# Kernel tuning notes

Measured on AMD Instinct MI355X. Metric: run time of the kernel, lower is better.

The kernel has to match this reference:

```python
import math
import jax, jax.numpy as jnp
import numpy as np
from jax import lax

B, C, H, W = 4, 256, 64, 64
TD = 256
GROUPS = 32
EPS = 1e-5


def group_norm(x, scale, bias, groups=GROUPS, eps=EPS):
    b, c, h, w = x.shape
    xg = x.reshape(b, groups, c // groups, h, w)
    m = xg.mean(axis=(2, 3, 4), keepdims=True)
    v = xg.var(axis=(2, 3, 4), keepdims=True)
    xn = ((xg - m) * lax.rsqrt(v + eps)).reshape(b, c, h, w)
    return xn * scale[None, :, None, None] + bias[None, :, None, None]


def conv3x3(x, w, b):
    y = lax.conv_general_dilated(x, w, (1, 1), 'SAME',
                                 dimension_numbers=('NCHW', 'OIHW', 'NCHW'))
    return y + b[None, :, None, None]


def setup_inputs() -> dict:
    key = jax.random.key(0)
    ks = jax.random.split(key, 10)
    s = 0.02
    return {
        'x': jax.random.normal(ks[0], (B, C, H, W), jnp.float32),
        'time_embed': jax.random.normal(ks[1], (B, TD), jnp.float32),
        # ResNetBlock params
        'gn1_s': jnp.ones((C,), jnp.float32), 'gn1_b': jnp.zeros((C,), jnp.float32),
        'conv1_w': jax.random.normal(ks[2], (C, C, 3, 3), jnp.float32) * s,
        'conv1_b': jnp.zeros((C,), jnp.float32),
        'mlp_w': jax.random.normal(ks[3], (2 * C, TD), jnp.float32) * s,
        'mlp_b': jnp.zeros((2 * C,), jnp.float32),
        'gn2_s': jnp.ones((C,), jnp.float32), 'gn2_b': jnp.zeros((C,), jnp.float32),
        'conv2_w': jax.random.normal(ks[4], (C, C, 3, 3), jnp.float32) * s,
        'conv2_b': jnp.zeros((C,), jnp.float32),
        # SelfAttention params (n_head=1, 1x1 convs stored as matrices)
        'gnA_s': jnp.ones((C,), jnp.float32), 'gnA_b': jnp.zeros((C,), jnp.float32),
        'qkv_w': jax.random.normal(ks[5], (3 * C, C), jnp.float32) * s,
        'out_w': jax.random.normal(ks[6], (C, C), jnp.float32) * s,
        'out_b': jnp.zeros((C,), jnp.float32),
    }


def reference(x, time_embed, gn1_s, gn1_b, conv1_w, conv1_b, mlp_w, mlp_b,
              gn2_s, gn2_b, conv2_w, conv2_b, gnA_s, gnA_b, qkv_w, out_w, out_b):
    # --- ResNetBlock ---
    h = conv3x3(jax.nn.silu(group_norm(x, gn1_s, gn1_b)), conv1_w, conv1_b)
    # time-embedding FiLM: SiLU -> Linear -> (gamma, beta)
    gb = jnp.dot(jax.nn.silu(time_embed), mlp_w.T) + mlp_b  # [B, 2C]
    gamma, beta = jnp.split(gb[:, :, None, None], 2, axis=1)
    h = (1.0 + gamma) * h + beta
    h = conv3x3(jax.nn.silu(group_norm(h, gn2_s, gn2_b)), conv2_w, conv2_b)
    xr = h + x  # res_conv is Identity since dim == dim_out

    # --- SelfAttention (n_head=1, scale = sqrt(channel)) ---
    b, c, hh, ww = xr.shape
    n = group_norm(xr, gnA_s, gnA_b)
    qkv = jnp.einsum('oc,bchw->bohw', qkv_w, n)  # [B, 3C, H, W]
    q, k, v = jnp.split(qkv.reshape(b, 3 * c, hh * ww), 3, axis=1)  # [B,C,HW] each
    attn = jnp.einsum('bcs,bct->bst', q, k) / math.sqrt(c)  # [B, HW, HW]
    attn = jax.nn.softmax(attn, axis=-1)
    o = jnp.einsum('bst,bct->bcs', attn, v).reshape(b, c, hh, ww)
    o = jnp.einsum('oc,bchw->bohw', out_w, o) + out_b[None, :, None, None]
    return o + xr
```

## Files before the change

kernel.cpp:

```cpp
#include <hip/hip_runtime.h>
#include <math.h>

#define SS 4096
#define NE 4194304

typedef __attribute__((ext_vector_type(8))) short short8;
typedef __attribute__((ext_vector_type(4))) short short4v;
typedef __attribute__((ext_vector_type(4))) float f32x4;
typedef __attribute__((ext_vector_type(16))) float f32x16;

__device__ __forceinline__ float wave_sum(float v) {
#pragma unroll
  for (int off = 32; off > 0; off >>= 1) v += __shfl_xor(v, off, 64);
  return v;
}
__device__ __forceinline__ float silu_f(float y) { return y / (1.f + __expf(-y)); }

__device__ __forceinline__ unsigned short to_bf(float x) {
  union { float f; unsigned u; } v; v.f = x;
  unsigned r = v.u + 0x7FFFu + ((v.u >> 16) & 1u);
  return (unsigned short)(r >> 16);
}
__device__ __forceinline__ float bf2f(short s) {
  union { unsigned u; float f; } v;
  v.u = ((unsigned)(unsigned short)s) << 16;
  return v.f;
}

__global__ __launch_bounds__(256) void gn_stats_k(const float* __restrict__ x,
                                                  float* __restrict__ stats) {
  const float4* p = (const float4*)(x + (size_t)blockIdx.x * 32768);
  float s = 0.f, q = 0.f;
  for (int i = threadIdx.x; i < 8192; i += 256) {
    float4 v = p[i];
    s += v.x + v.y + v.z + v.w;
    q += v.x * v.x + v.y * v.y + v.z * v.z + v.w * v.w;
  }
  s = wave_sum(s); q = wave_sum(q);
  __shared__ float red[8];
  int wid = threadIdx.x >> 6;
  if ((threadIdx.x & 63) == 0) { red[wid] = s; red[wid + 4] = q; }
  __syncthreads();
  if (threadIdx.x == 0) {
    s = red[0] + red[1] + red[2] + red[3];
    q = red[4] + red[5] + red[6] + red[7];
    float m = s * (1.f / 32768.f);
    float var = q * (1.f / 32768.f) - m * m;
    stats[blockIdx.x * 2] = m;
    stats[blockIdx.x * 2 + 1] = rsqrtf(var + 1e-5f);
  }
}

template <int DO_SILU>
__global__ __launch_bounds__(256) void gn_t_k(const float* __restrict__ x,
    const float* __restrict__ stats, const float* __restrict__ sc,
    const float* __restrict__ bi, short* __restrict__ G) {
  __shared__ short T[64][72];
  const int tid = threadIdx.x;
  const int st = blockIdx.x & 63;
  const int ct = (blockIdx.x >> 6) & 3;
  const int b = blockIdx.x >> 8;
  const int s0 = st * 64, c0 = ct * 64;
#pragma unroll
  for (int r = 0; r < 4; ++r) {
    int idx = r * 256 + tid;
    int c_l = idx >> 4, s4 = idx & 15;
    int c = c0 + c_l;
    int sidx = (b * 32 + (c >> 3)) * 2;
    float m = stats[sidx], rs = stats[sidx + 1];
    float a = sc[c] * rs;
    float t = bi[c] - m * a;
    float4 v = *(const float4*)(x + ((size_t)(b * 256 + c)) * 4096 + s0 + s4 * 4);
    float o0 = v.x * a + t, o1 = v.y * a + t, o2 = v.z * a + t, o3 = v.w * a + t;
    if (DO_SILU) { o0 = silu_f(o0); o1 = silu_f(o1); o2 = silu_f(o2); o3 = silu_f(o3); }
    T[s4 * 4 + 0][c_l] = (short)to_bf(o0);
    T[s4 * 4 + 1][c_l] = (short)to_bf(o1);
    T[s4 * 4 + 2][c_l] = (short)to_bf(o2);
    T[s4 * 4 + 3][c_l] = (short)to_bf(o3);
  }
  __syncthreads();
#pragma unroll
  for (int r = 0; r < 2; ++r) {
    int idx = r * 256 + tid;
    int s_l = idx >> 3, cg = idx & 7;
    *(short8*)(G + ((size_t)(b * 4096 + s0 + s_l)) * 256 + c0 + cg * 8) =
        *(const short8*)&T[s_l][cg * 8];
  }
}

__global__ __launch_bounds__(256) void prep_k(
    const float* __restrict__ conv1_w, const float* __restrict__ conv2_w,
    const float* __restrict__ qkv_w, const float* __restrict__ out_w,
    const float* __restrict__ te, const float* __restrict__ mlp_w,
    const float* __restrict__ mlp_b, short* __restrict__ Wt1,
    short* __restrict__ Wt2, short* __restrict__ wqb, short* __restrict__ wob,
    float* __restrict__ gbuf) {
  const int bid = blockIdx.x, tid = threadIdx.x;
  if (bid < 512) {
    __shared__ short L[9][256];
    const float* w = (bid < 256) ? conv1_w : conv2_w;
    short* wt = (bid < 256) ? Wt1 : Wt2;
    const int oc = bid & 255;
    const float* wp = w + (size_t)oc * 2304;
    for (int i = tid; i < 2304; i += 256) {
      int ic = i / 9, t = i - ic * 9;
      L[t][ic] = (short)to_bf(wp[i]);
    }
    __syncthreads();
    for (int i = tid; i < 2304; i += 256) {
      int t = i >> 8, ic = i & 255;
      wt[((size_t)(t * 256 + oc)) * 256 + ic] = L[t][ic];
    }
  } else if (bid < 1280) {
    int row = bid - 512;
    float sc = (row < 256) ? 0.0625f : 1.f;
    wqb[(size_t)row * 256 + tid] = (short)to_bf(qkv_w[(size_t)row * 256 + tid] * sc);
  } else if (bid < 1536) {
    int row = bid - 1280;
    wob[(size_t)row * 256 + tid] = (short)to_bf(out_w[(size_t)row * 256 + tid]);
  } else {
    int t2 = (bid - 1536) * 256 + tid;
    int b = t2 >> 9, jj = t2 & 511;
    const float* tp = te + b * 256;
    const float* wp = mlp_w + jj * 256;
    float acc = mlp_b[jj];
    for (int t = 0; t < 256; ++t) acc += silu_f(tp[t]) * wp[t];
    gbuf[t2] = acc;
  }
}

__device__ __forceinline__ short8 ld2x4(const short* p) {
  short4v lo = *(const short4v*)p;
  short4v hi = *(const short4v*)(p + 4);
  short8 r;
  r[0] = lo[0]; r[1] = lo[1]; r[2] = lo[2]; r[3] = lo[3];
  r[4] = hi[0]; r[5] = hi[1]; r[6] = hi[2]; r[7] = hi[3];
  return r;
}

template <int MODE>
__global__ __launch_bounds__(256, 1) void conv_mfma_k(
    const short* __restrict__ G, const short* __restrict__ Wt,
    const float* __restrict__ bias, const float* __restrict__ gb,
    const float* __restrict__ resid, float* __restrict__ out) {
  __shared__ __align__(16) short Xs[6][66][36];
  __shared__ __align__(16) short Ws[9][64][32];
  const int tid = threadIdx.x;
  const int oc0 = (blockIdx.x & 3) * 64;
  const int oy = ((blockIdx.x >> 2) & 15) * 4;
  const int b = blockIdx.x >> 6;
  const int wv = tid >> 6, lane = tid & 63;
  const int ln = lane & 31, hf = lane >> 5;

  f32x16 O00 = {}, O01 = {}, O10 = {}, O11 = {};

  for (int ic0 = 0; ic0 < 256; ic0 += 32) {
    __syncthreads();
    for (int i = tid; i < 1584; i += 256) {
      int r = i / 264;
      int rem = i - r * 264;
      int col = rem >> 2, g = rem & 3;
      int gy = oy + r - 1, gx = col - 1;
      short4v lo = {0, 0, 0, 0}, hi = {0, 0, 0, 0};
      if ((unsigned)gy < 64u && (unsigned)gx < 64u) {
        const short* gp = G + ((size_t)(b * 4096 + gy * 64 + gx)) * 256 + ic0 + g * 8;
        lo = *(const short4v*)gp;
        hi = *(const short4v*)(gp + 4);
      }
      *(short4v*)&Xs[r][col][g * 8] = lo;
      *(short4v*)&Xs[r][col][g * 8 + 4] = hi;
    }
    for (int i = tid; i < 2304; i += 256) {
      int t = i >> 8;
      int rem = i & 255;
      int o = rem >> 2, g = rem & 3;
      *(short8*)&Ws[t][o][g * 8] =
          *(const short8*)(Wt + ((size_t)(t * 256 + oc0 + o)) * 256 + ic0 + g * 8);
    }
    __syncthreads();
    for (int t = 0; t < 9; ++t) {
      const int dy = t / 3, dx = t - dy * 3;
      const short* xrow = &Xs[wv + dy][0][0];
#pragma unroll
      for (int ks = 0; ks < 2; ++ks) {
        short8 a0 = *(const short8*)&Ws[t][ln][ks * 16 + hf * 8];
        short8 a1 = *(const short8*)&Ws[t][32 + ln][ks * 16 + hf * 8];
        short8 b0 = ld2x4(xrow + (ln + dx) * 36 + ks * 16 + hf * 8);
        short8 b1 = ld2x4(xrow + (32 + ln + dx) * 36 + ks * 16 + hf * 8);
        O00 = __builtin_amdgcn_mfma_f32_32x32x16_bf16(a0, b0, O00, 0, 0, 0);
        O01 = __builtin_amdgcn_mfma_f32_32x32x16_bf16(a0, b1, O01, 0, 0, 0);
        O10 = __builtin_amdgcn_mfma_f32_32x32x16_bf16(a1, b0, O10, 0, 0, 0);
        O11 = __builtin_amdgcn_mfma_f32_32x32x16_bf16(a1, b1, O11, 0, 0, 0);
      }
    }
  }
  const int srow = (oy + wv) * 64;
#pragma unroll
  for (int os = 0; os < 2; ++os) {
    const f32x16* Oa = os ? &O10 : &O00;
    const f32x16* Ob = os ? &O11 : &O01;
#pragma unroll
    for (int i = 0; i < 16; ++i) {
      int oc = oc0 + os * 32 + (i & 3) + 8 * (i >> 2) + 4 * hf;
      float bi = bias[oc];
      size_t base = ((size_t)(b * 256 + oc)) * 4096 + srow;
      float v0 = (*Oa)[i] + bi, v1 = (*Ob)[i] + bi;
      if (MODE == 0) {
        float ga = 1.f + gb[b * 512 + oc], be = gb[b * 512 + 256 + oc];
        v0 = ga * v0 + be;
        v1 = ga * v1 + be;
      } else {
        v0 += resid[base + ln];
        v1 += resid[base + 32 + ln];
      }
      out[base + ln] = v0;
      out[base + 32 + ln] = v1;
    }
  }
}

template <int MODE>
__global__ __launch_bounds__(256, 2) void gemm1x1_k(
    const short* __restrict__ X, const short* __restrict__ W,
    const float* __restrict__ bias, const float* __restrict__ ml,
    short* __restrict__ q, short* __restrict__ k, short* __restrict__ v,
    float* __restrict__ out) {
  __shared__ __align__(16) short sh[18432];
  const int tid = threadIdx.x;
  const int o0 = blockIdx.x * 64;
  const int s0 = blockIdx.y * 256;
  const int b = blockIdx.z;
  const int w = tid >> 6, lane = tid & 63, ln = lane & 31, hf = lane >> 5;
  {
    const int o = tid >> 2, g = tid & 3;
#pragma unroll
    for (int j = 0; j < 8; ++j) {
      int c = (g * 8 + j) * 8;
      *(short8*)&sh[o * 264 + c] = *(const short8*)(W + (size_t)(o0 + o) * 256 + c);
    }
  }
  __syncthreads();
  f32x16 acc[2][2] = {{{}, {}}, {{}, {}}};
  if (MODE == 0) {
    const short* xp = X + ((size_t)(b * 4096 + s0 + w * 64)) * 256;
    short8 bf0 = *(const short8*)(xp + (size_t)ln * 256 + hf * 8);
    short8 bf1 = *(const short8*)(xp + (size_t)(32 + ln) * 256 + hf * 8);
#pragma unroll
    for (int ks = 0; ks < 16; ++ks) {
      short8 a0 = *(const short8*)&sh[ln * 264 + ks * 16 + hf * 8];
      short8 a1 = *(const short8*)&sh[(32 + ln) * 264 + ks * 16 + hf * 8];
      short8 nb0 = bf0, nb1 = bf1;
      if (ks < 15) {
        nb0 = *(const short8*)(xp + (size_t)ln * 256 + (ks + 1) * 16 + hf * 8);
        nb1 = *(const short8*)(xp + (size_t)(32 + ln) * 256 + (ks + 1) * 16 + hf * 8);
      }
      acc[0][0] = __builtin_amdgcn_mfma_f32_32x32x16_bf16(a0, bf0, acc[0][0], 0, 0, 0);
      acc[0][1] = __builtin_amdgcn_mfma_f32_32x32x16_bf16(a0, bf1, acc[0][1], 0, 0, 0);
      acc[1][0] = __builtin_amdgcn_mfma_f32_32x32x16_bf16(a1, bf0, acc[1][0], 0, 0, 0);
      acc[1][1] = __builtin_amdgcn_mfma_f32_32x32x16_bf16(a1, bf1, acc[1][1], 0, 0, 0);
      bf0 = nb0; bf1 = nb1;
    }
  } else {
    const size_t r0 = (size_t)b * 4096 + s0 + w * 64 + ln;
    const size_t r1 = r0 + 32;
    float inv0 = 1.f / (ml[r0] + ml[16384 + r0] + ml[32768 + r0] + ml[49152 + r0]);
    float inv1 = 1.f / (ml[r1] + ml[16384 + r1] + ml[32768 + r1] + ml[49152 + r1]);
#pragma unroll 4
    for (int ks = 0; ks < 16; ++ks) {
      float t0[8] = {0, 0, 0, 0, 0, 0, 0, 0}, t1[8] = {0, 0, 0, 0, 0, 0, 0, 0};
#pragma unroll
      for (int z = 0; z < 4; ++z) {
        short8 p0 = *(const short8*)(X + ((size_t)z * 16384 + r0) * 256 + ks * 16 + hf * 8);
        short8 p1 = *(const short8*)(X + ((size_t)z * 16384 + r1) * 256 + ks * 16 + hf * 8);
#pragma unroll
        for (int jj = 0; jj < 8; ++jj) { t0[jj] += bf2f(p0[jj]); t1[jj] += bf2f(p1[jj]); }
      }
      short8 bf0, bf1;
#pragma unroll
      for (int jj = 0; jj < 8; ++jj) {
        bf0[jj] = (short)to_bf(t0[jj] * inv0);
        bf1[jj] = (short)to_bf(t1[jj] * inv1);
      }
      short8 a0 = *(const short8*)&sh[ln * 264 + ks * 16 + hf * 8];
      short8 a1 = *(const short8*)&sh[(32 + ln) * 264 + ks * 16 + hf * 8];
      acc[0][0] = __builtin_amdgcn_mfma_f32_32x32x16_bf16(a0, bf0, acc[0][0], 0, 0, 0);
      acc[0][1] = __builtin_amdgcn_mfma_f32_32x32x16_bf16(a0, bf1, acc[0][1], 0, 0, 0);
      acc[1][0] = __builtin_amdgcn_mfma_f32_32x32x16_bf16(a1, bf0, acc[1][0], 0, 0, 0);
      acc[1][1] = __builtin_amdgcn_mfma_f32_32x32x16_bf16(a1, bf1, acc[1][1], 0, 0, 0);
    }
  }
  if (MODE == 1) {
#pragma unroll
    for (int os = 0; os < 2; ++os)
#pragma unroll
      for (int ss = 0; ss < 2; ++ss)
#pragma unroll
        for (int i = 0; i < 16; ++i) {
          int oc = o0 + os * 32 + (i & 3) + 8 * (i >> 2) + 4 * hf;
          size_t idx = ((size_t)(b * 256 + oc)) * 4096 + s0 + w * 64 + ss * 32 + ln;
          out[idx] = out[idx] + acc[os][ss][i] + bias[oc];
        }
  } else if (o0 >= 512) {
#pragma unroll
    for (int os = 0; os < 2; ++os)
#pragma unroll
      for (int ss = 0; ss < 2; ++ss)
#pragma unroll
        for (int i = 0; i < 16; ++i) {
          int oc = (o0 - 512) + os * 32 + (i & 3) + 8 * (i >> 2) + 4 * hf;
          v[((size_t)(b * 256 + oc)) * 4096 + s0 + w * 64 + ss * 32 + ln] =
              (short)to_bf(acc[os][ss][i]);
        }
  } else {
    __syncthreads();
#pragma unroll
    for (int os = 0; os < 2; ++os)
#pragma unroll
      for (int ss = 0; ss < 2; ++ss)
#pragma unroll
        for (int i = 0; i < 16; ++i) {
          int o_l = os * 32 + (i & 3) + 8 * (i >> 2) + 4 * hf;
          int s_l = ss * 32 + ln;
          sh[(w * 64 + s_l) * 72 + o_l] = (short)to_bf(acc[os][ss][i]);
        }
    __syncthreads();
    short* dst = (o0 < 256) ? q : k;
    const int co = (o0 < 256) ? o0 : o0 - 256;
    const short* src = &sh[(w * 64 + lane) * 72];
    short* gp = dst + ((size_t)(b * 4096 + s0 + w * 64 + lane)) * 256 + co;
#pragma unroll
    for (int j = 0; j < 8; ++j)
      *(short8*)(gp + j * 8) = *(const short8*)(src + j * 8);
  }
}

__global__ __launch_bounds__(256, 2) void attn_k(const short* __restrict__ qb,
    const short* __restrict__ kb, const short* __restrict__ vb,
    short* __restrict__ part, float* __restrict__ ml) {
  __shared__ __align__(16) short qls[64 * 268];
  __shared__ __align__(16) short vls[256 * 68];
  __shared__ __align__(16) short pls[64 * 68];
  __shared__ __align__(16) float lss[64 * 4];
  const int tid = threadIdx.x;
  const int j = blockIdx.x & 7;
  const int b = j >> 1;
  const int idx = ((blockIdx.x >> 3) << 1) | (j & 1);
  const int z = idx >> 6;
  const int s0 = (idx & 63) * 64;
  const int kv0 = z * 1024;
  const int w = tid >> 6, lane = tid & 63, ln = lane & 15, qd = lane >> 4;

  {
    const short* qsrc = qb + ((size_t)(b * 4096 + s0)) * 256;
    for (int i = tid; i < 2048; i += 256) {
      int r = i >> 5, cc = i & 31;
      *(short8*)&qls[r * 268 + cc * 8] = *(const short8*)(qsrc + (size_t)r * 256 + cc * 8);
    }
  }
  const f32x4 z4 = {0.f, 0.f, 0.f, 0.f};
  f32x4 O[4][4];
#pragma unroll
  for (int g = 0; g < 4; ++g)
#pragma unroll
    for (int cs = 0; cs < 4; ++cs) O[g][cs] = z4;
  float l_loc[4] = {0.f, 0.f, 0.f, 0.f};

  const short* kbb = kb + ((size_t)(b * 4096 + kv0)) * 256;
  const short* vbb = vb + ((size_t)b * 256) * 4096 + kv0;

  const int vr = tid >> 3;
  const int vc = (tid & 7) * 8;

  short8 kreg[8], vreg[8];
#pragma unroll
  for (int ks = 0; ks < 8; ++ks)
    kreg[ks] = *(const short8*)(kbb + ((size_t)(w * 16 + ln)) * 256 + ks * 32 + qd * 8);
#pragma unroll
  for (int p = 0; p < 8; ++p)
    vreg[p] = *(const short8*)(vbb + ((size_t)(vr + p * 32)) * 4096 + vc);
  __syncthreads();

  for (int t0 = 0; t0 < 1024; t0 += 64) {
    const int tn = (t0 + 64 < 1024) ? t0 + 64 : t0;
#pragma unroll
    for (int p = 0; p < 8; ++p)
      *(short8*)&vls[(vr + p * 32) * 68 + vc] = vreg[p];
#pragma unroll
    for (int p = 0; p < 8; ++p)
      vreg[p] = *(const short8*)(vbb + ((size_t)(vr + p * 32)) * 4096 + tn + vc);
    f32x4 S[4] = {z4, z4, z4, z4};
#pragma unroll
    for (int ks = 0; ks < 8; ++ks) {
#pragma unroll
      for (int g = 0; g < 4; ++g) {
        short8 qf = *(const short8*)&qls[(g * 16 + ln) * 268 + ks * 32 + qd * 8];
        S[g] = __builtin_amdgcn_mfma_f32_16x16x32_bf16(kreg[ks], qf, S[g], 0, 0, 0);
      }
    }
#pragma unroll
    for (int ks = 0; ks < 8; ++ks)
      kreg[ks] = *(const short8*)(kbb + ((size_t)(tn + w * 16 + ln)) * 256 + ks * 32 + qd * 8);
#pragma unroll
    for (int g = 0; g < 4; ++g) {
      const int q = g * 16 + ln;
      float p0 = __expf(S[g][0]), p1 = __expf(S[g][1]);
      float p2 = __expf(S[g][2]), p3 = __expf(S[g][3]);
      unsigned lo = (unsigned)to_bf(p0) | ((unsigned)to_bf(p1) << 16);
      unsigned hi = (unsigned)to_bf(p2) | ((unsigned)to_bf(p3) << 16);
      *(unsigned*)&pls[q * 68 + w * 16 + qd * 4] = lo;
      *(unsigned*)&pls[q * 68 + w * 16 + qd * 4 + 2] = hi;
      l_loc[g] += (p0 + p1) + (p2 + p3);
    }
    __syncthreads();
#pragma unroll
    for (int kc = 0; kc < 2; ++kc) {
      short8 pf[4];
#pragma unroll
      for (int g = 0; g < 4; ++g)
        pf[g] = *(const short8*)&pls[(g * 16 + ln) * 68 + kc * 32 + qd * 8];
#pragma unroll
      for (int cs = 0; cs < 4; ++cs) {
        short8 vf = *(const short8*)&vls[(w * 64 + cs * 16 + ln) * 68 + kc * 32 + qd * 8];
#pragma unroll
        for (int g = 0; g < 4; ++g)
          O[g][cs] = __builtin_amdgcn_mfma_f32_16x16x32_bf16(vf, pf[g], O[g][cs], 0, 0, 0);
      }
    }
    __syncthreads();
  }
#pragma unroll
  for (int g = 0; g < 4; ++g) {
    float lg = l_loc[g];
    lg += __shfl_xor(lg, 16, 64);
    lg += __shfl_xor(lg, 32, 64);
    if (qd == 0) lss[(g * 16 + ln) * 4 + w] = lg;
  }
  __syncthreads();
  const size_t prow = (size_t)z * 16384 + (size_t)b * 4096 + s0;
#pragma unroll
  for (int g = 0; g < 4; ++g) {
    short* pp = part + (prow + g * 16 + ln) * 256 + w * 64 + qd * 4;
#pragma unroll
    for (int cs = 0; cs < 4; ++cs) {
      short4v o4;
      o4[0] = (short)to_bf(O[g][cs][0]);
      o4[1] = (short)to_bf(O[g][cs][1]);
      o4[2] = (short)to_bf(O[g][cs][2]);
      o4[3] = (short)to_bf(O[g][cs][3]);
      *(short4v*)(pp + cs * 16) = o4;
    }
  }
  if (w == 0 && qd == 0) {
#pragma unroll
    for (int g = 0; g < 4; ++g) {
      const int q = g * 16 + ln;
      f32x4 lt = *(const f32x4*)&lss[q * 4];
      ml[(size_t)z * 16384 + (size_t)b * 4096 + s0 + q] =
          (lt[0] + lt[1]) + (lt[2] + lt[3]);
    }
  }
}

extern "C" void kernel_launch(void* const* d_in, const int* in_sizes, int n_in,
                              void* d_out, int out_size, void* d_ws, size_t ws_size,
                              hipStream_t stream) {
  const float* x       = (const float*)d_in[0];
  const float* te      = (const float*)d_in[1];
  const float* gn1_s   = (const float*)d_in[2];
  const float* gn1_b   = (const float*)d_in[3];
  const float* conv1_w = (const float*)d_in[4];
  const float* conv1_b = (const float*)d_in[5];
  const float* mlp_w   = (const float*)d_in[6];
  const float* mlp_b   = (const float*)d_in[7];
  const float* gn2_s   = (const float*)d_in[8];
  const float* gn2_b   = (const float*)d_in[9];
  const float* conv2_w = (const float*)d_in[10];
  const float* conv2_b = (const float*)d_in[11];
  const float* gnA_s   = (const float*)d_in[12];
  const float* gnA_b   = (const float*)d_in[13];
  const float* qkv_w   = (const float*)d_in[14];
  const float* out_w   = (const float*)d_in[15];
  const float* out_b   = (const float*)d_in[16];
  float* out = (float*)d_out;

  float* bufA  = (float*)d_ws;
  float* bufB  = bufA + NE;
  short* qb    = (short*)(bufB + NE);
  short* kb    = qb + NE;
  short* vb    = kb + NE;
  float* mlb   = (float*)(vb + NE);
  float* stats = mlb + 65536;
  float* gbuf  = stats + 768;
  short* wqb   = (short*)(gbuf + 2048);
  short* wob   = wqb + 196608;
  short* G     = qb;
  short* Wt1   = kb;
  short* Wt2   = Wt1 + 589824;
  short* nT    = (short*)bufA;
  short* partb = (short*)bufA;

  prep_k<<<1544, 256, 0, stream>>>(conv1_w, conv2_w, qkv_w, out_w, te, mlp_w,
                                   mlp_b, Wt1, Wt2, wqb, wob, gbuf);
  gn_stats_k<<<128, 256, 0, stream>>>(x, stats);
  gn_t_k<1><<<1024, 256, 0, stream>>>(x, stats, gn1_s, gn1_b, G);
  conv_mfma_k<0><<<256, 256, 0, stream>>>(G, Wt1, conv1_b, gbuf, nullptr, bufB);
  gn_stats_k<<<128, 256, 0, stream>>>(bufB, stats + 256);
  gn_t_k<1><<<1024, 256, 0, stream>>>(bufB, stats + 256, gn2_s, gn2_b, G);
  conv_mfma_k<1><<<256, 256, 0, stream>>>(G, Wt2, conv2_b, nullptr, x, out);
  gn_stats_k<<<128, 256, 0, stream>>>(out, stats + 512);
  gn_t_k<0><<<1024, 256, 0, stream>>>(out, stats + 512, gnA_s, gnA_b, nT);
  gemm1x1_k<0><<<dim3(12, 16, 4), 256, 0, stream>>>(nT, wqb, nullptr, nullptr,
                                                    qb, kb, vb, nullptr);
  attn_k<<<1024, 256, 0, stream>>>(qb, kb, vb, partb, mlb);
  gemm1x1_k<1><<<dim3(4, 16, 4), 256, 0, stream>>>(partb, wob, out_b, mlb,
                                                   nullptr, nullptr, nullptr, out);
}
```

Before: 413.6 us.

## Switch attention kernel to 32x32x16 MFMA and feed V directly from registers

Rewrites the attention inner loop to use 32x32x16 bf16 MFMA tiles. Each wave computes a 32x32 score block and a 64-channel by 64-query output block. V fragments are loaded from global memory straight into MFMA operand registers, so the V staging buffer in LDS and its store pass are gone. This cuts LDS traffic and shared memory use, which may allow more blocks per CU. The cost is larger per-wave accumulators (four f32x16) and more K registers, which raises register pressure, and the V global loads are strided per lane.

```diff
diff --git a/kernel.cpp b/kernel.cpp
--- a/kernel.cpp
+++ b/kernel.cpp
@@ -338,7 +338,6 @@
     const short* __restrict__ kb, const short* __restrict__ vb,
     short* __restrict__ part, float* __restrict__ ml) {
   __shared__ __align__(16) short qls[64 * 268];
-  __shared__ __align__(16) short vls[256 * 68];
   __shared__ __align__(16) short pls[64 * 68];
   __shared__ __align__(16) float lss[64 * 4];
   const int tid = threadIdx.x;
@@ -348,7 +347,9 @@
   const int z = idx >> 6;
   const int s0 = (idx & 63) * 64;
   const int kv0 = z * 1024;
-  const int w = tid >> 6, lane = tid & 63, ln = lane & 15, qd = lane >> 4;
+  const int w = tid >> 6, lane = tid & 63;
+  const int ln = lane & 31, hf = lane >> 5;
+  const int qh = w >> 1, kh = w & 1;
 
   {
     const short* qsrc = qb + ((size_t)(b * 4096 + s0)) * 256;
@@ -357,107 +358,86 @@
       *(short8*)&qls[r * 268 + cc * 8] = *(const short8*)(qsrc + (size_t)r * 256 + cc * 8);
     }
   }
-  const f32x4 z4 = {0.f, 0.f, 0.f, 0.f};
-  f32x4 O[4][4];
-#pragma unroll
-  for (int g = 0; g < 4; ++g)
-#pragma unroll
-    for (int cs = 0; cs < 4; ++cs) O[g][cs] = z4;
-  float l_loc[4] = {0.f, 0.f, 0.f, 0.f};
+  f32x16 O00 = {}, O01 = {}, O10 = {}, O11 = {};
+  float l_loc = 0.f;
 
   const short* kbb = kb + ((size_t)(b * 4096 + kv0)) * 256;
   const short* vbb = vb + ((size_t)b * 256) * 4096 + kv0;
 
-  const int vr = tid >> 3;
-  const int vc = (tid & 7) * 8;
-
-  short8 kreg[8], vreg[8];
-#pragma unroll
-  for (int ks = 0; ks < 8; ++ks)
-    kreg[ks] = *(const short8*)(kbb + ((size_t)(w * 16 + ln)) * 256 + ks * 32 + qd * 8);
-#pragma unroll
-  for (int p = 0; p < 8; ++p)
-    vreg[p] = *(const short8*)(vbb + ((size_t)(vr + p * 32)) * 4096 + vc);
+  short8 kreg[16], vreg[8];
+#pragma unroll
+  for (int ks = 0; ks < 16; ++ks)
+    kreg[ks] = *(const short8*)(kbb + ((size_t)(kh * 32 + ln)) * 256 + ks * 16 + hf * 8);
+#pragma unroll
+  for (int i = 0; i < 8; ++i)
+    vreg[i] = *(const short8*)(vbb + ((size_t)(w * 64 + (i >> 2) * 32 + ln)) * 4096 +
+                               (i & 3) * 16 + hf * 8);
   __syncthreads();
 
   for (int t0 = 0; t0 < 1024; t0 += 64) {
     const int tn = (t0 + 64 < 1024) ? t0 + 64 : t0;
-#pragma unroll
-    for (int p = 0; p < 8; ++p)
-      *(short8*)&vls[(vr + p * 32) * 68 + vc] = vreg[p];
-#pragma unroll
-    for (int p = 0; p < 8; ++p)
-      vreg[p] = *(const short8*)(vbb + ((size_t)(vr + p * 32)) * 4096 + tn + vc);
-    f32x4 S[4] = {z4, z4, z4, z4};
-#pragma unroll
-    for (int ks = 0; ks < 8; ++ks) {
-#pragma unroll
-      for (int g = 0; g < 4; ++g) {
-        short8 qf = *(const short8*)&qls[(g * 16 + ln) * 268 + ks * 32 + qd * 8];
-        S[g] = __builtin_amdgcn_mfma_f32_16x16x32_bf16(kreg[ks], qf, S[g], 0, 0, 0);
-      }
-    }
-#pragma unroll
-    for (int ks = 0; ks < 8; ++ks)
-      kreg[ks] = *(const short8*)(kbb + ((size_t)(tn + w * 16 + ln)) * 256 + ks * 32 + qd * 8);
-#pragma unroll
-    for (int g = 0; g < 4; ++g) {
-      const int q = g * 16 + ln;
-      float p0 = __expf(S[g][0]), p1 = __expf(S[g][1]);
-      float p2 = __expf(S[g][2]), p3 = __expf(S[g][3]);
-      unsigned lo = (unsigned)to_bf(p0) | ((unsigned)to_bf(p1) << 16);
-      unsigned hi = (unsigned)to_bf(p2) | ((unsigned)to_bf(p3) << 16);
-      *(unsigned*)&pls[q * 68 + w * 16 + qd * 4] = lo;
-      *(unsigned*)&pls[q * 68 + w * 16 + qd * 4 + 2] = hi;
-      l_loc[g] += (p0 + p1) + (p2 + p3);
-    }
-    __syncthreads();
-#pragma unroll
-    for (int kc = 0; kc < 2; ++kc) {
-      short8 pf[4];
-#pragma unroll
-      for (int g = 0; g < 4; ++g)
-        pf[g] = *(const short8*)&pls[(g * 16 + ln) * 68 + kc * 32 + qd * 8];
-#pragma unroll
-      for (int cs = 0; cs < 4; ++cs) {
-        short8 vf = *(const short8*)&vls[(w * 64 + cs * 16 + ln) * 68 + kc * 32 + qd * 8];
-#pragma unroll
-        for (int g = 0; g < 4; ++g)
-          O[g][cs] = __builtin_amdgcn_mfma_f32_16x16x32_bf16(vf, pf[g], O[g][cs], 0, 0, 0);
-      }
-    }
-    __syncthreads();
-  }
-#pragma unroll
-  for (int g = 0; g < 4; ++g) {
-    float lg = l_loc[g];
-    lg += __shfl_xor(lg, 16, 64);
-    lg += __shfl_xor(lg, 32, 64);
-    if (qd == 0) lss[(g * 16 + ln) * 4 + w] = lg;
+    f32x16 S = {};
+#pragma unroll
+    for (int ks = 0; ks < 16; ++ks) {
+      short8 qf = *(const short8*)&qls[(qh * 32 + ln) * 268 + ks * 16 + hf * 8];
+      S = __builtin_amdgcn_mfma_f32_32x32x16_bf16(kreg[ks], qf, S, 0, 0, 0);
+    }
+#pragma unroll
+    for (int ks = 0; ks < 16; ++ks)
+      kreg[ks] = *(const short8*)(kbb + ((size_t)(tn + kh * 32 + ln)) * 256 + ks * 16 + hf * 8);
+    __syncthreads();
+#pragma unroll
+    for (int r2 = 0; r2 < 4; ++r2) {
+      float p0 = __expf(S[r2 * 4 + 0]), p1 = __expf(S[r2 * 4 + 1]);
+      float p2 = __expf(S[r2 * 4 + 2]), p3 = __expf(S[r2 * 4 + 3]);
+      short4v p4;
+      p4[0] = (short)to_bf(p0); p4[1] = (short)to_bf(p1);
+      p4[2] = (short)to_bf(p2); p4[3] = (short)to_bf(p3);
+      *(short4v*)&pls[(qh * 32 + ln) * 68 + kh * 32 + hf * 4 + r2 * 8] = p4;
+      l_loc += (p0 + p1) + (p2 + p3);
+    }
+    __syncthreads();
+#pragma unroll
+    for (int k2 = 0; k2 < 4; ++k2) {
+      short8 pf0 = *(const short8*)&pls[ln * 68 + k2 * 16 + hf * 8];
+      short8 pf1 = *(const short8*)&pls[(32 + ln) * 68 + k2 * 16 + hf * 8];
+      O00 = __builtin_amdgcn_mfma_f32_32x32x16_bf16(vreg[k2], pf0, O00, 0, 0, 0);
+      O01 = __builtin_amdgcn_mfma_f32_32x32x16_bf16(vreg[k2], pf1, O01, 0, 0, 0);
+      O10 = __builtin_amdgcn_mfma_f32_32x32x16_bf16(vreg[4 + k2], pf0, O10, 0, 0, 0);
+      O11 = __builtin_amdgcn_mfma_f32_32x32x16_bf16(vreg[4 + k2], pf1, O11, 0, 0, 0);
+    }
+#pragma unroll
+    for (int i = 0; i < 8; ++i)
+      vreg[i] = *(const short8*)(vbb + ((size_t)(w * 64 + (i >> 2) * 32 + ln)) * 4096 +
+                                 tn + (i & 3) * 16 + hf * 8);
+  }
+  {
+    float lg = l_loc + __shfl_xor(l_loc, 32, 64);
+    if (hf == 0) lss[(qh * 32 + ln) * 4 + kh] = lg;
   }
   __syncthreads();
   const size_t prow = (size_t)z * 16384 + (size_t)b * 4096 + s0;
 #pragma unroll
-  for (int g = 0; g < 4; ++g) {
-    short* pp = part + (prow + g * 16 + ln) * 256 + w * 64 + qd * 4;
-#pragma unroll
-    for (int cs = 0; cs < 4; ++cs) {
-      short4v o4;
-      o4[0] = (short)to_bf(O[g][cs][0]);
-      o4[1] = (short)to_bf(O[g][cs][1]);
-      o4[2] = (short)to_bf(O[g][cs][2]);
-      o4[3] = (short)to_bf(O[g][cs][3]);
-      *(short4v*)(pp + cs * 16) = o4;
-    }
-  }
-  if (w == 0 && qd == 0) {
-#pragma unroll
-    for (int g = 0; g < 4; ++g) {
-      const int q = g * 16 + ln;
-      f32x4 lt = *(const f32x4*)&lss[q * 4];
-      ml[(size_t)z * 16384 + (size_t)b * 4096 + s0 + q] =
-          (lt[0] + lt[1]) + (lt[2] + lt[3]);
-    }
+  for (int ca = 0; ca < 2; ++ca) {
+    const f32x16* Oa = ca ? &O10 : &O00;
+    const f32x16* Ob = ca ? &O11 : &O01;
+#pragma unroll
+    for (int r2 = 0; r2 < 4; ++r2) {
+      int cb = w * 64 + ca * 32 + 4 * hf + 8 * r2;
+      short4v oa4, ob4;
+#pragma unroll
+      for (int r1 = 0; r1 < 4; ++r1) {
+        oa4[r1] = (short)to_bf((*Oa)[r2 * 4 + r1]);
+        ob4[r1] = (short)to_bf((*Ob)[r2 * 4 + r1]);
+      }
+      *(short4v*)(part + (prow + ln) * 256 + cb) = oa4;
+      *(short4v*)(part + (prow + 32 + ln) * 256 + cb) = ob4;
+    }
+  }
+  if (w == 0) {
+    int q = lane;
+    ml[(size_t)z * 16384 + (size_t)b * 4096 + s0 + q] =
+        lss[q * 4 + 0] + lss[q * 4 + 1];
   }
 }
 
```

Result: slower. 517.6 us (+25.1%).
